# Optimization experiments

Hardware: AMD Instinct MI355X
Metric: run time of the kernel (lower is better)

Reference implementation:

```python
import jax, jax.numpy as jnp
import numpy as np

B, A, D, H = 16384, 4096, 512, 512
BIN_SIZE = 0.05
EPS = 1e-12


def _l2_normalize(t):
    # matches torch F.normalize(p=2, dim=-1): x / max(||x||, eps)
    n = jnp.sqrt(jnp.sum(t * t, axis=-1, keepdims=True))
    return t / jnp.maximum(n, EPS)


def setup_inputs() -> dict:
    key = jax.random.key(0)
    k1, k2, k3, k4, k5 = jax.random.split(key, 5)
    x = jax.random.normal(k1, (B, D), dtype=jnp.float32)
    anchors = jax.random.normal(k2, (A, D), dtype=jnp.float32)
    # nn.Linear(D, H, bias=False) weights, shape [H, D]
    s = 1.0 / np.sqrt(D)
    W_q = jax.random.uniform(k3, (H, D), dtype=jnp.float32, minval=-s, maxval=s)
    W_k = jax.random.uniform(k4, (H, D), dtype=jnp.float32, minval=-s, maxval=s)
    # trainable values: [n_anchors, hidden_features]
    values = jax.random.normal(k5, (A, H), dtype=jnp.float32)
    return {"x": x, "anchors": anchors, "W_q": W_q, "W_k": W_k, "values": values}


def reference(x, anchors, W_q, W_k, values):
    # per-element linear transforms (queries / keys), no bias
    q = x @ W_q.T          # [B, H]
    k = anchors @ W_k.T    # [A, H]
    # NormalizationMode.L2
    q = _l2_normalize(q)
    k = _l2_normalize(k)
    # RelativeEmbeddingMethod.INNER (no 1/sqrt(d) since normalization is on)
    similarities = jnp.einsum('bm,am->ba', q, k)  # [B, A]
    # SimilaritiesQuantizationMode.DIFFERENTIABLE_ROUND (straight-through)
    rounded = jnp.round(similarities / BIN_SIZE) * BIN_SIZE
    quantized = similarities + jax.lax.stop_gradient(rounded - similarities)
    # ValuesMethod.TRAINABLE: softmax-weighted combination of trainable values
    weights = jax.nn.softmax(quantized, axis=-1)  # [B, A]
    output = jnp.einsum('bw,wh->bh', weights, values)  # [B, H]
    return output, similarities
```

## Files before the change

kernel.cpp:

```cpp
#include <hip/hip_runtime.h>
#include <hip/hip_bf16.h>


#define B_N 16384
#define A_N 4096
#define D_N 512
#define H_N 512

typedef __attribute__((ext_vector_type(8))) short bf16x8;
typedef __attribute__((ext_vector_type(4))) float f32x4;

__device__ __forceinline__ short f2bf(float f) {
  union { float f; unsigned int u; } v;
  v.f = f;
  unsigned int r = v.u + 0x7FFFu + ((v.u >> 16) & 1u);
  return (short)(r >> 16);
}
__device__ __forceinline__ float bf2f(short s) {
  union { float f; unsigned int u; } v;
  v.u = ((unsigned int)(unsigned short)s) << 16;
  return v.f;
}

__device__ __forceinline__ void async_copy16(const void* g, void* l) {
  __builtin_amdgcn_global_load_lds(
      (const __attribute__((address_space(1))) unsigned int*)g,
      (__attribute__((address_space(3))) unsigned int*)l, 16, 0, 0);
}

__global__ void convert_w_kernel(const float* __restrict__ W, short* __restrict__ out) {
  int u = blockIdx.x * 256 + threadIdx.x;
  int row = u >> 6;
  int cu = u & 63;
  const float4* src = (const float4*)(W + (size_t)row * 512 + cu * 8);
  float4 a = src[0], b = src[1];
  bf16x8 o;
  o[0]=f2bf(a.x); o[1]=f2bf(a.y); o[2]=f2bf(a.z); o[3]=f2bf(a.w);
  o[4]=f2bf(b.x); o[5]=f2bf(b.y); o[6]=f2bf(b.z); o[7]=f2bf(b.w);
  int cu2 = cu ^ (row & 7);
  *(bf16x8*)(out + (size_t)row * 512 + cu2 * 8) = o;
}

__global__ void transpose_values_kernel(const float* __restrict__ vals, short* __restrict__ vt) {
  __shared__ float tile[64][65];
  int t = threadIdx.x;
  int a0 = (blockIdx.x & 63) * 64;
  int h0 = (blockIdx.x >> 6) * 64;
#pragma unroll
  for (int r = 0; r < 4; ++r) {
    int ar = r * 16 + (t >> 4);
    int hc = (t & 15) * 4;
    float4 v = *(const float4*)(vals + (size_t)(a0 + ar) * 512 + h0 + hc);
    tile[ar][hc + 0] = v.x; tile[ar][hc + 1] = v.y;
    tile[ar][hc + 2] = v.z; tile[ar][hc + 3] = v.w;
  }
  __syncthreads();
#pragma unroll
  for (int r = 0; r < 2; ++r) {
    int u = r * 256 + t;
    int hr = u >> 3;
    int cu = u & 7;
    int h = h0 + hr;
    bf16x8 o;
#pragma unroll
    for (int j = 0; j < 8; ++j) o[j] = f2bf(tile[cu * 8 + j][hr]);
    int cu2 = cu ^ (h & 7);
    *(bf16x8*)(vt + (size_t)h * 4096 + a0 + cu2 * 8) = o;
  }
}

template <int SWZ>
__global__ __launch_bounds__(256, 2) void proj_norm_kernel(
    const float* __restrict__ X, const short* __restrict__ Wcv, short* __restrict__ out) {
  __shared__ __align__(16) short xs[64 * 64];
  __shared__ __align__(16) short wsb[512 * 64];
  const int t = threadIdx.x;
  const int lane = t & 63;
  const int wv = t >> 6;
  const int l15 = lane & 15;
  const int lhi = lane >> 4;
  const int row0 = blockIdx.x * 64;

  const f32x4 ZZ = {0.f, 0.f, 0.f, 0.f};
  f32x4 acc[32];
#pragma unroll
  for (int i = 0; i < 32; ++i) acc[i] = ZZ;

  for (int kc = 0; kc < 8; ++kc) {
    const int k0 = kc * 64;
#pragma unroll
    for (int i = 0; i < 2; ++i) {
      int u = i * 256 + t;
      int row = u >> 3, cu = u & 7;
      const float4* src = (const float4*)(X + (size_t)(row0 + row) * 512 + k0 + cu * 8);
      float4 a = src[0], b = src[1];
      bf16x8 o;
      o[0]=f2bf(a.x); o[1]=f2bf(a.y); o[2]=f2bf(a.z); o[3]=f2bf(a.w);
      o[4]=f2bf(b.x); o[5]=f2bf(b.y); o[6]=f2bf(b.z); o[7]=f2bf(b.w);
      *(bf16x8*)(&xs[row * 64 + ((cu ^ (row & 7)) * 8)]) = o;
    }
#pragma unroll
    for (int i = 0; i < 16; ++i) {
      int u = i * 256 + t;
      async_copy16((const char*)Wcv + (size_t)(u >> 3) * 1024 + k0 * 2 + (u & 7) * 16,
                   (char*)wsb + u * 16);
    }
    __syncthreads();

    bf16x8 af[2];
    const int arow = wv * 16 + l15;
#pragma unroll
    for (int kk = 0; kk < 2; ++kk)
      af[kk] = *(const bf16x8*)(&xs[arow * 64 + (((kk * 4 + lhi) ^ (arow & 7)) * 8)]);
#pragma unroll
    for (int nt = 0; nt < 32; ++nt) {
      const int brow = nt * 16 + l15;
      const int bs = brow & 7;
#pragma unroll
      for (int kk = 0; kk < 2; ++kk) {
        bf16x8 bf = *(const bf16x8*)(&wsb[brow * 64 + (((kk * 4 + lhi) ^ bs) * 8)]);
        acc[nt] = __builtin_amdgcn_mfma_f32_16x16x32_bf16(af[kk], bf, acc[nt], 0, 0, 0);
      }
    }
    __syncthreads();
  }

  float ssq[4] = {0.f, 0.f, 0.f, 0.f};
#pragma unroll
  for (int nt = 0; nt < 32; ++nt)
#pragma unroll
    for (int r = 0; r < 4; ++r) ssq[r] += acc[nt][r] * acc[nt][r];
#pragma unroll
  for (int r = 0; r < 4; ++r) {
    ssq[r] += __shfl_xor(ssq[r], 1);
    ssq[r] += __shfl_xor(ssq[r], 2);
    ssq[r] += __shfl_xor(ssq[r], 4);
    ssq[r] += __shfl_xor(ssq[r], 8);
  }
  float scale[4];
#pragma unroll
  for (int r = 0; r < 4; ++r) scale[r] = 1.0f / fmaxf(sqrtf(ssq[r]), 1e-12f);

#pragma unroll
  for (int nt = 0; nt < 32; ++nt) {
#pragma unroll
    for (int r = 0; r < 4; ++r) {
      int grow = row0 + wv * 16 + lhi * 4 + r;
      int col = nt * 16 + l15;
      int ocol = SWZ ? (col ^ ((grow & 7) << 3)) : col;
      out[(size_t)grow * 512 + ocol] = f2bf(acc[nt][r] * scale[r]);
    }
  }
}

__global__ __launch_bounds__(512, 2) void attn_kernel(
    const short* __restrict__ qn,
    const short* __restrict__ kn,
    const short* __restrict__ vt,
    float* __restrict__ outp,
    float* __restrict__ sims) {
  __shared__ __align__(16) short ks[64 * 512];
  __shared__ __align__(16) short vs[512 * 64];
  __shared__ __align__(16) short wsm[64 * 64];
  __shared__ __align__(16) float sbuf[64 * 68];
  __shared__ float sums[64];

  const int tid = threadIdx.x;
  const int lane = tid & 63;
  const int wid = tid >> 6;
  const int l15 = lane & 15;
  const int lhi = lane >> 4;
  const int b0 = blockIdx.x * 64;
  const int ag = wid >> 1;
  const int bg = wid & 1;

  if (tid < 64) sums[tid] = 0.0f;

  bf16x8 qf[2][16];
#pragma unroll
  for (int tt = 0; tt < 2; ++tt) {
    const short* qp = qn + (size_t)(b0 + bg * 32 + tt * 16 + l15) * 512 + lhi * 8;
#pragma unroll
    for (int k = 0; k < 16; ++k) qf[tt][k] = *(const bf16x8*)(qp + k * 32);
  }

  const f32x4 ZZ = {0.f, 0.f, 0.f, 0.f};
  f32x4 accO[4][4];
#pragma unroll
  for (int i = 0; i < 4; ++i)
#pragma unroll
    for (int j = 0; j < 4; ++j) accO[i][j] = ZZ;
  float sum_p0 = 0.f, sum_p1 = 0.f;

  auto stage_k = [&](int cc) {
    const size_t kb = (size_t)cc * 64 * 1024;
#pragma unroll
    for (int i = 0; i < 8; ++i) {
      int u = i * 512 + tid;
      async_copy16((const char*)kn + kb + (size_t)(u >> 6) * 1024 + (u & 63) * 16,
                   (char*)ks + u * 16);
    }
  };
  auto stage_v = [&](int cc) {
    const size_t vb = (size_t)cc * 128;
#pragma unroll
    for (int i = 0; i < 8; ++i) {
      int u = i * 512 + tid;
      async_copy16((const char*)vt + (size_t)(u >> 3) * 8192 + vb + (u & 7) * 16,
                   (char*)vs + u * 16);
    }
  };

  stage_k(0);
  stage_v(0);

  for (int c = 0; c < 64; ++c) {
    const int c0 = c * 64;
    __syncthreads();

    f32x4 sAcc[2] = {ZZ, ZZ};
    const int arow = ag * 16 + l15;
    const int asw = arow & 7;
#pragma unroll
    for (int k = 0; k < 16; ++k) {
      bf16x8 kf = *(const bf16x8*)(&ks[arow * 512 + (((k * 4 + lhi) ^ asw) * 8)]);
#pragma unroll
      for (int tt = 0; tt < 2; ++tt)
        sAcc[tt] = __builtin_amdgcn_mfma_f32_16x16x32_bf16(kf, qf[tt][k], sAcc[tt], 0, 0, 0);
    }

#pragma unroll
    for (int tt = 0; tt < 2; ++tt) {
      const int brow = bg * 32 + tt * 16 + l15;
      const int bsw = (brow & 7) << 3;
      float lsum = 0.f;
#pragma unroll
      for (int r = 0; r < 4; ++r) {
        const int aloc = ag * 16 + lhi * 4 + r;
        float s = sAcc[tt][r];
        sbuf[brow * 68 + aloc] = s;
        float rv = rintf(s * 20.0f) * 0.05f;
        float wv = __expf(rv);
        short wb = f2bf(wv);
        wsm[brow * 64 + (aloc ^ bsw)] = wb;
        lsum += bf2f(wb);
      }
      if (tt == 0) sum_p0 += lsum; else sum_p1 += lsum;
    }
    __syncthreads();

    if (c + 1 < 64) stage_k(c + 1);

    {
      const int row = tid >> 3;
      const int seg = tid & 7;
      const float* sp = &sbuf[row * 68 + seg * 8];
      float4 v0 = *(const float4*)sp;
      float4 v1 = *(const float4*)(sp + 4);
      float4* gp = (float4*)(sims + (size_t)(b0 + row) * 4096 + c0 + seg * 8);
      gp[0] = v0;
      gp[1] = v1;
    }

#pragma unroll
    for (int kk = 0; kk < 2; ++kk) {
      bf16x8 wf[4];
#pragma unroll
      for (int bt = 0; bt < 4; ++bt) {
        const int br = bt * 16 + l15;
        wf[bt] = *(const bf16x8*)(&wsm[br * 64 + (((kk * 4 + lhi) ^ (br & 7)) * 8)]);
      }
#pragma unroll
      for (int ht = 0; ht < 4; ++ht) {
        const int hr = wid * 64 + ht * 16 + l15;
        bf16x8 vf = *(const bf16x8*)(&vs[hr * 64 + (((kk * 4 + lhi) ^ (hr & 7)) * 8)]);
#pragma unroll
        for (int bt = 0; bt < 4; ++bt)
          accO[ht][bt] = __builtin_amdgcn_mfma_f32_16x16x32_bf16(vf, wf[bt], accO[ht][bt], 0, 0, 0);
      }
    }
    __syncthreads();

    if (c + 1 < 64) stage_v(c + 1);
  }

  sum_p0 += __shfl_xor(sum_p0, 16);
  sum_p0 += __shfl_xor(sum_p0, 32);
  sum_p1 += __shfl_xor(sum_p1, 16);
  sum_p1 += __shfl_xor(sum_p1, 32);
  if (lane < 16) {
    atomicAdd(&sums[bg * 32 + lane], sum_p0);
    atomicAdd(&sums[bg * 32 + 16 + lane], sum_p1);
  }
  __syncthreads();

#pragma unroll
  for (int bt = 0; bt < 4; ++bt) {
    const int b = bt * 16 + l15;
    const float inv = 1.0f / sums[b];
#pragma unroll
    for (int ht = 0; ht < 4; ++ht) {
      f32x4 o = accO[ht][bt];
      float4 st;
      st.x = o[0] * inv; st.y = o[1] * inv; st.z = o[2] * inv; st.w = o[3] * inv;
      *(float4*)(outp + (size_t)(b0 + b) * 512 + wid * 64 + ht * 16 + lhi * 4) = st;
    }
  }
}

extern "C" void kernel_launch(void* const* d_in, const int* in_sizes, int n_in,
                              void* d_out, int out_size, void* d_ws, size_t ws_size,
                              hipStream_t stream) {
  const float* x       = (const float*)d_in[0];
  const float* anchors = (const float*)d_in[1];
  const float* Wq      = (const float*)d_in[2];
  const float* Wk      = (const float*)d_in[3];
  const float* values  = (const float*)d_in[4];

  float* out  = (float*)d_out;
  float* sims = out + (size_t)B_N * H_N;

  char* ws = (char*)d_ws;
  short* q_bf  = (short*)(ws);
  short* k_bf  = (short*)(ws + (16u << 20));
  short* vt_bf = (short*)(ws + (20u << 20));
  short* wq_cv = (short*)(ws + (24u << 20));
  short* wk_cv = (short*)(ws + (24u << 20) + (512u << 10));

  convert_w_kernel<<<128, 256, 0, stream>>>(Wq, wq_cv);
  convert_w_kernel<<<128, 256, 0, stream>>>(Wk, wk_cv);
  transpose_values_kernel<<<512, 256, 0, stream>>>(values, vt_bf);
  proj_norm_kernel<0><<<B_N / 64, 256, 0, stream>>>(x, wq_cv, q_bf);
  proj_norm_kernel<1><<<A_N / 64, 256, 0, stream>>>(anchors, wk_cv, k_bf);
  attn_kernel<<<B_N / 64, 512, 0, stream>>>(q_bf, k_bf, vt_bf, out, sims);
}
```

Measured before the change: 745.9 us.

## Double-buffer K tiles, load V from global into registers, write sims directly

The attention kernel now double-buffers the K tile in LDS, prefetching two chunks ahead. It drops the V staging buffer: V is stored in a chunk-contiguous pre-swizzled layout so each wave loads its V fragments straight from global memory into registers. Similarity scores go to global directly from the MFMA accumulators instead of through an LDS staging buffer, and barriers are replaced with raw s_barrier plus explicit waitcnt. The two weight conversions are merged into one launch. The aim is to cut LDS traffic and barrier stalls and overlap loads with MFMA work, at the cost of uncoalesced sims stores, more register pressure, and reliance on hand-placed waitcnts for correctness.

```diff
diff --git a/kernel.cpp b/kernel.cpp
--- a/kernel.cpp
+++ b/kernel.cpp
@@ -8,6 +8,7 @@
 #define H_N 512
 
 typedef __attribute__((ext_vector_type(8))) short bf16x8;
+typedef __attribute__((ext_vector_type(4))) short s16x4;
 typedef __attribute__((ext_vector_type(4))) float f32x4;
 
 __device__ __forceinline__ short f2bf(float f) {
@@ -28,24 +29,42 @@
       (__attribute__((address_space(3))) unsigned int*)l, 16, 0, 0);
 }
 
-__global__ void convert_w_kernel(const float* __restrict__ W, short* __restrict__ out) {
-  int u = blockIdx.x * 256 + threadIdx.x;
+#define BARRIER_LGKM() do {                                   \
+    asm volatile("s_waitcnt lgkmcnt(0)" ::: "memory");        \
+    __builtin_amdgcn_s_barrier();                             \
+    __builtin_amdgcn_sched_barrier(0);                        \
+    asm volatile("" ::: "memory");                            \
+  } while (0)
+#define BARRIER_PLAIN() do {                                  \
+    asm volatile("" ::: "memory");                            \
+    __builtin_amdgcn_s_barrier();                             \
+    __builtin_amdgcn_sched_barrier(0);                        \
+    asm volatile("" ::: "memory");                            \
+  } while (0)
+
+__global__ void convert_w_kernel(const float* __restrict__ Wq, const float* __restrict__ Wk,
+                                 short* __restrict__ oq, short* __restrict__ ok) {
+  const int b = blockIdx.x;
+  const float* W = (b < 128) ? Wq : Wk;
+  short* out = (b < 128) ? oq : ok;
+  int u = (b & 127) * 256 + threadIdx.x;
   int row = u >> 6;
   int cu = u & 63;
   const float4* src = (const float4*)(W + (size_t)row * 512 + cu * 8);
-  float4 a = src[0], b = src[1];
+  float4 a = src[0], bb = src[1];
   bf16x8 o;
   o[0]=f2bf(a.x); o[1]=f2bf(a.y); o[2]=f2bf(a.z); o[3]=f2bf(a.w);
-  o[4]=f2bf(b.x); o[5]=f2bf(b.y); o[6]=f2bf(b.z); o[7]=f2bf(b.w);
+  o[4]=f2bf(bb.x); o[5]=f2bf(bb.y); o[6]=f2bf(bb.z); o[7]=f2bf(bb.w);
   int cu2 = cu ^ (row & 7);
   *(bf16x8*)(out + (size_t)row * 512 + cu2 * 8) = o;
 }
 
-__global__ void transpose_values_kernel(const float* __restrict__ vals, short* __restrict__ vt) {
+__global__ void transpose_values_kernel(const float* __restrict__ vals, short* __restrict__ vtc) {
   __shared__ float tile[64][65];
   int t = threadIdx.x;
-  int a0 = (blockIdx.x & 63) * 64;
+  int c  = blockIdx.x & 63;
   int h0 = (blockIdx.x >> 6) * 64;
+  int a0 = c * 64;
 #pragma unroll
   for (int r = 0; r < 4; ++r) {
     int ar = r * 16 + (t >> 4);
@@ -59,13 +78,12 @@
   for (int r = 0; r < 2; ++r) {
     int u = r * 256 + t;
     int hr = u >> 3;
-    int cu = u & 7;
-    int h = h0 + hr;
+    int au = u & 7;
     bf16x8 o;
 #pragma unroll
-    for (int j = 0; j < 8; ++j) o[j] = f2bf(tile[cu * 8 + j][hr]);
-    int cu2 = cu ^ (h & 7);
-    *(bf16x8*)(vt + (size_t)h * 4096 + a0 + cu2 * 8) = o;
+    for (int j = 0; j < 8; ++j) o[j] = f2bf(tile[au * 8 + j][hr]);
+    int au2 = au ^ (hr & 7);
+    *(bf16x8*)(vtc + (size_t)c * 32768 + (size_t)(h0 + hr) * 64 + au2 * 8) = o;
   }
 }
 
@@ -156,13 +174,11 @@
 __global__ __launch_bounds__(512, 2) void attn_kernel(
     const short* __restrict__ qn,
     const short* __restrict__ kn,
-    const short* __restrict__ vt,
+    const short* __restrict__ vtc,
     float* __restrict__ outp,
     float* __restrict__ sims) {
-  __shared__ __align__(16) short ks[64 * 512];
-  __shared__ __align__(16) short vs[512 * 64];
-  __shared__ __align__(16) short wsm[64 * 64];
-  __shared__ __align__(16) float sbuf[64 * 68];
+  __shared__ __align__(16) short ks[2][64 * 512];
+  __shared__ __align__(16) short wsm[64 * 72];
   __shared__ float sums[64];
 
   const int tid = threadIdx.x;
@@ -192,74 +208,79 @@
     for (int j = 0; j < 4; ++j) accO[i][j] = ZZ;
   float sum_p0 = 0.f, sum_p1 = 0.f;
 
-  auto stage_k = [&](int cc) {
-    const size_t kb = (size_t)cc * 64 * 1024;
+  auto stage_k = [&](int cc, int bufi) {
+    const char* src = (const char*)kn + (size_t)cc * 65536;
+    char* dst = (char*)&ks[bufi][0];
 #pragma unroll
     for (int i = 0; i < 8; ++i) {
       int u = i * 512 + tid;
-      async_copy16((const char*)kn + kb + (size_t)(u >> 6) * 1024 + (u & 63) * 16,
-                   (char*)ks + u * 16);
+      async_copy16(src + u * 16, dst + u * 16);
     }
   };
-  auto stage_v = [&](int cc) {
-    const size_t vb = (size_t)cc * 128;
-#pragma unroll
-    for (int i = 0; i < 8; ++i) {
-      int u = i * 512 + tid;
-      async_copy16((const char*)vt + (size_t)(u >> 3) * 8192 + vb + (u & 7) * 16,
-                   (char*)vs + u * 16);
-    }
-  };
-
-  stage_k(0);
-  stage_v(0);
+
+  stage_k(0, 0);
+  stage_k(1, 1);
+  asm volatile("s_waitcnt vmcnt(0) lgkmcnt(0)" ::: "memory");
+  __builtin_amdgcn_s_barrier();
+  __builtin_amdgcn_sched_barrier(0);
+
+  const int arow = ag * 16 + l15;
+  const int asw = arow & 7;
 
   for (int c = 0; c < 64; ++c) {
-    const int c0 = c * 64;
-    __syncthreads();
+    const short* ksb = &ks[c & 1][0];
+
+    bf16x8 vbuf[8];
+    {
+      const char* vbase = (const char*)vtc + (size_t)c * 65536 + (size_t)wid * 8192;
+#pragma unroll
+      for (int kk = 0; kk < 2; ++kk)
+#pragma unroll
+        for (int ht = 0; ht < 4; ++ht) {
+          int hr = ht * 16 + l15;
+          vbuf[kk * 4 + ht] =
+              *(const bf16x8*)(vbase + hr * 128 + (((kk * 4 + lhi) ^ (l15 & 7)) * 16));
+        }
+    }
 
     f32x4 sAcc[2] = {ZZ, ZZ};
-    const int arow = ag * 16 + l15;
-    const int asw = arow & 7;
 #pragma unroll
     for (int k = 0; k < 16; ++k) {
-      bf16x8 kf = *(const bf16x8*)(&ks[arow * 512 + (((k * 4 + lhi) ^ asw) * 8)]);
+      bf16x8 kf = *(const bf16x8*)(&ksb[arow * 512 + (((k * 4 + lhi) ^ asw) * 8)]);
 #pragma unroll
       for (int tt = 0; tt < 2; ++tt)
         sAcc[tt] = __builtin_amdgcn_mfma_f32_16x16x32_bf16(kf, qf[tt][k], sAcc[tt], 0, 0, 0);
     }
 
+    const int aloc0 = ag * 16 + lhi * 4;
 #pragma unroll
     for (int tt = 0; tt < 2; ++tt) {
       const int brow = bg * 32 + tt * 16 + l15;
-      const int bsw = (brow & 7) << 3;
+      const int scol = aloc0 ^ ((brow & 7) << 3);
+      s16x4 w4;
       float lsum = 0.f;
 #pragma unroll
       for (int r = 0; r < 4; ++r) {
-        const int aloc = ag * 16 + lhi * 4 + r;
-        float s = sAcc[tt][r];
-        sbuf[brow * 68 + aloc] = s;
-        float rv = rintf(s * 20.0f) * 0.05f;
-        float wv = __expf(rv);
-        short wb = f2bf(wv);
-        wsm[brow * 64 + (aloc ^ bsw)] = wb;
+        float rv = rintf(sAcc[tt][r] * 20.0f) * 0.05f;
+        short wb = f2bf(__expf(rv));
+        w4[r] = wb;
         lsum += bf2f(wb);
       }
+      *(s16x4*)(&wsm[brow * 72 + scol]) = w4;
       if (tt == 0) sum_p0 += lsum; else sum_p1 += lsum;
     }
-    __syncthreads();
-
-    if (c + 1 < 64) stage_k(c + 1);
+
+    BARRIER_LGKM();
 
     {
-      const int row = tid >> 3;
-      const int seg = tid & 7;
-      const float* sp = &sbuf[row * 68 + seg * 8];
-      float4 v0 = *(const float4*)sp;
-      float4 v1 = *(const float4*)(sp + 4);
-      float4* gp = (float4*)(sims + (size_t)(b0 + row) * 4096 + c0 + seg * 8);
-      gp[0] = v0;
-      gp[1] = v1;
+      int cs = c + 2; if (cs > 63) cs = 63;
+      stage_k(cs, c & 1);
+    }
+
+#pragma unroll
+    for (int tt = 0; tt < 2; ++tt) {
+      const int brow = bg * 32 + tt * 16 + l15;
+      *(f32x4*)(sims + (size_t)(b0 + brow) * 4096 + c * 64 + aloc0) = sAcc[tt];
     }
 
 #pragma unroll
@@ -268,26 +289,25 @@
 #pragma unroll
       for (int bt = 0; bt < 4; ++bt) {
         const int br = bt * 16 + l15;
-        wf[bt] = *(const bf16x8*)(&wsm[br * 64 + (((kk * 4 + lhi) ^ (br & 7)) * 8)]);
+        wf[bt] = *(const bf16x8*)(&wsm[br * 72 + (((kk * 4 + lhi) ^ (br & 7)) * 8)]);
       }
 #pragma unroll
       for (int ht = 0; ht < 4; ++ht) {
-        const int hr = wid * 64 + ht * 16 + l15;
-        bf16x8 vf = *(const bf16x8*)(&vs[hr * 64 + (((kk * 4 + lhi) ^ (hr & 7)) * 8)]);
 #pragma unroll
         for (int bt = 0; bt < 4; ++bt)
-          accO[ht][bt] = __builtin_amdgcn_mfma_f32_16x16x32_bf16(vf, wf[bt], accO[ht][bt], 0, 0, 0);
+          accO[ht][bt] = __builtin_amdgcn_mfma_f32_16x16x32_bf16(
+              vbuf[kk * 4 + ht], wf[bt], accO[ht][bt], 0, 0, 0);
       }
     }
-    __syncthreads();
-
-    if (c + 1 < 64) stage_v(c + 1);
+
+    BARRIER_PLAIN();
   }
 
   sum_p0 += __shfl_xor(sum_p0, 16);
   sum_p0 += __shfl_xor(sum_p0, 32);
   sum_p1 += __shfl_xor(sum_p1, 16);
   sum_p1 += __shfl_xor(sum_p1, 32);
+  __syncthreads();
   if (lane < 16) {
     atomicAdd(&sums[bg * 32 + lane], sum_p0);
     atomicAdd(&sums[bg * 32 + 16 + lane], sum_p1);
@@ -327,8 +347,7 @@
   short* wq_cv = (short*)(ws + (24u << 20));
   short* wk_cv = (short*)(ws + (24u << 20) + (512u << 10));
 
-  convert_w_kernel<<<128, 256, 0, stream>>>(Wq, wq_cv);
-  convert_w_kernel<<<128, 256, 0, stream>>>(Wk, wk_cv);
+  convert_w_kernel<<<256, 256, 0, stream>>>(Wq, Wk, wq_cv, wk_cv);
   transpose_values_kernel<<<512, 256, 0, stream>>>(values, vt_bf);
   proj_norm_kernel<0><<<B_N / 64, 256, 0, stream>>>(x, wq_cv, q_bf);
   proj_norm_kernel<1><<<A_N / 64, 256, 0, stream>>>(anchors, wk_cv, k_bf);
```

Result: slower. 815.4 us (+9.3%).
